# Performance work log

Measured on AMD Instinct MI355X. Metric: run time of the kernel, lower is better.

Reference implementation:

```python
import jax, jax.numpy as jnp
import numpy as np

NEG = jnp.float32(-1e30)  # max-plus identity (finite to keep grads clean)


def setup_inputs() -> dict:
    key = jax.random.key(0)
    k1, k2 = jax.random.split(key)
    B, Cin, H, W = 8, 64, 64, 64
    Cout, kH, kW = 64, 3, 3
    x = jax.random.normal(k1, (B, Cin, H, W), dtype=jnp.float32)
    weight = jax.random.normal(k2, (Cout, Cin, kH, kW), dtype=jnp.float32)
    return {"x": x, "weight": weight, "kernel_size": 3, "padding": 1}


def reference(x, weight, kernel_size, padding):
    # Max-plus correlation (tropical conv), stride 1:
    #   out[b,co,y,x] = max_{ci,i,j} ( x_pad[b,ci,y+i,x+j] + weight[co,ci,i,j] )
    kH = kW = int(kernel_size)
    padH = padW = int(padding)
    B, Cin, H, W = x.shape
    Cout = weight.shape[0]
    xp = jnp.pad(x, ((0, 0), (0, 0), (padH, padH), (padW, padW)),
                 constant_values=NEG)  # -inf-like padding: identity of max
    Ho = H + 2 * padH - kH + 1
    Wo = W + 2 * padW - kW + 1
    out = jnp.full((B, Cout, Ho, Wo), NEG, dtype=x.dtype)
    for i in range(kH):          # small fixed kernel loop (kH*kW taps)
        for j in range(kW):
            win = xp[:, :, i:i + Ho, j:j + Wo]            # [B,Ci,Ho,Wo]
            cand = win[:, None] + weight[None, :, :, i, j, None, None]
            out = jnp.maximum(out, cand.max(axis=2))      # reduce over Ci
    return out
```

## Files before the change

### kernel.cpp

```cpp
#include <hip/hip_runtime.h>

#define NEGV -1e30f

constexpr int Bn = 8, Ci = 64, Hn = 64, Wn = 64, Co = 64;

constexpr int COB = 8;
constexpr int HT  = 4;

__global__ __launch_bounds__(256, 4)
void maxconv_kernel(const float* __restrict__ x, const float* __restrict__ wt,
                    float* __restrict__ out) {
    const int lane = threadIdx.x & 63;
    const int wrow = threadIdx.x >> 6;
    const int co0  = blockIdx.x * COB;
    const int h    = blockIdx.y * HT + wrow;
    const int b    = blockIdx.z;

    const int cl = lane > 0      ? lane - 1 : 0;
    const int cr = lane < Wn - 1 ? lane + 1 : Wn - 1;
    const bool edgeL = (lane == 0);
    const bool edgeR = (lane == Wn - 1);
    const bool hasUp = (h > 0);
    const bool hasDn = (h < Hn - 1);

    float acc[COB];
#pragma unroll
    for (int c = 0; c < COB; c++) acc[c] = NEGV;

    const float* p = x + ((size_t)b * Ci * Hn + h) * Wn;

    for (int ci = 0; ci < Ci; ci++, p += Hn * Wn) {
        float lm1 = NEGV, xm1 = NEGV, rm1 = NEGV;
        float lp1 = NEGV, xp1 = NEGV, rp1 = NEGV;
        if (hasUp) { lm1 = p[cl - Wn]; xm1 = p[lane - Wn]; rm1 = p[cr - Wn]; }
        if (hasDn) { lp1 = p[cl + Wn]; xp1 = p[lane + Wn]; rp1 = p[cr + Wn]; }
        float l0 = p[cl], x0 = p[lane], r0 = p[cr];

        if (edgeL) { lm1 = NEGV; l0 = NEGV; lp1 = NEGV; }
        if (edgeR) { rm1 = NEGV; r0 = NEGV; rp1 = NEGV; }

#pragma unroll
        for (int c = 0; c < COB; c++) {
            const float* wp = wt + ((size_t)(co0 + c) * Ci + ci) * 9;
            float t0 = lm1 + wp[0];
            float t1 = xm1 + wp[1];
            float t2 = rm1 + wp[2];
            float t3 = l0  + wp[3];
            float t4 = x0  + wp[4];
            float t5 = r0  + wp[5];
            float t6 = lp1 + wp[6];
            float t7 = xp1 + wp[7];
            float t8 = rp1 + wp[8];
            float a = acc[c];
            a = fmaxf(a, fmaxf(t0, t1));
            a = fmaxf(a, fmaxf(t2, t3));
            a = fmaxf(a, fmaxf(t4, t5));
            a = fmaxf(a, fmaxf(t6, t7));
            a = fmaxf(a, t8);
            acc[c] = a;
        }
    }

#pragma unroll
    for (int c = 0; c < COB; c++) {
        out[(((size_t)b * Co + co0 + c) * Hn + h) * Wn + lane] = acc[c];
    }
}

extern "C" void kernel_launch(void* const* d_in, const int* in_sizes, int n_in,
                              void* d_out, int out_size, void* d_ws, size_t ws_size,
                              hipStream_t stream) {
    const float* x  = (const float*)d_in[0];
    const float* wt = (const float*)d_in[1];
    float* out = (float*)d_out;

    dim3 grid(Co / COB, Hn / HT, Bn);
    maxconv_kernel<<<grid, 256, 0, stream>>>(x, wt, out);
}
```

Before: 125.4 us.

## Rewrite max-plus conv with weight pretranspose, double-buffered loads, max3 and XCD-aware grid

Adds a pre-pass kernel that repacks the weights so each channel group reads a contiguous block, plus a padding buffer of NEG values so the up and down border rows become branch-free pointer loads. The main kernel halves the channels per block to 4, software-pipelines the input and weight loads across pairs of input channels with sched barriers, reduces with v_max3_f32, and remaps block ids so that neighbouring blocks on one XCD share input rows. It also raises the occupancy hint. The cost is an extra kernel launch and twice as many blocks each re-reading the input.

```diff
diff --git a/kernel.cpp b/kernel.cpp
--- a/kernel.cpp
+++ b/kernel.cpp
@@ -4,67 +4,135 @@
 
 constexpr int Bn = 8, Ci = 64, Hn = 64, Wn = 64, Co = 64;
 
-constexpr int COB = 8;
-constexpr int HT  = 4;
+constexpr int COB = 4;
+constexpr int NG  = Co / COB;
+constexpr int WELEM = NG * Ci * COB * 9;
+constexpr int NEGN  = 64;
 
-__global__ __launch_bounds__(256, 4)
-void maxconv_kernel(const float* __restrict__ x, const float* __restrict__ wt,
-                    float* __restrict__ out) {
+__global__ __launch_bounds__(256)
+void wtrans_kernel(const float* __restrict__ wt, float* __restrict__ wT2) {
+    int idx = blockIdx.x * 256 + threadIdx.x;
+    if (idx < WELEM) {
+        int t  = idx % 36;
+        int cl = t / 9;
+        int k  = t % 9;
+        int ci = (idx / 36) % Ci;
+        int g  = idx / (36 * Ci);
+        wT2[idx] = wt[(((size_t)(g * COB + cl)) * Ci + ci) * 9 + k];
+    } else if (idx < WELEM + NEGN) {
+        wT2[idx] = NEGV;
+    }
+}
+
+__device__ __forceinline__ float vmax3(float a, float b, float c) {
+    float d;
+    asm("v_max3_f32 %0, %1, %2, %3" : "=v"(d) : "v"(a), "v"(b), "v"(c));
+    return d;
+}
+
+struct X9 { float um, uc, ur, cm, cc, cr, dm, dc, dr; };
+
+__device__ __forceinline__ void loadX(X9& x, const float* __restrict__ pu,
+                                      const float* __restrict__ pc,
+                                      const float* __restrict__ pd,
+                                      int cl, int lane, int cr2) {
+    x.um = pu[cl]; x.uc = pu[lane]; x.ur = pu[cr2];
+    x.cm = pc[cl]; x.cc = pc[lane]; x.cr = pc[cr2];
+    x.dm = pd[cl]; x.dc = pd[lane]; x.dr = pd[cr2];
+}
+
+__device__ __forceinline__ void edgefix(X9& x, bool eL, bool eR) {
+    x.um = eL ? NEGV : x.um;  x.cm = eL ? NEGV : x.cm;  x.dm = eL ? NEGV : x.dm;
+    x.ur = eR ? NEGV : x.ur;  x.cr = eR ? NEGV : x.cr;  x.dr = eR ? NEGV : x.dr;
+}
+
+__device__ __forceinline__ void loadW(float* wv, const float* __restrict__ base) {
+#pragma unroll
+    for (int j = 0; j < 36; j++) wv[j] = base[j];
+}
+
+__device__ __forceinline__ void computeC(float* acc, const X9& x, const float* wv) {
+#pragma unroll
+    for (int c = 0; c < COB; c++) {
+        const float* w = wv + c * 9;
+        float t0 = x.um + w[0], t1 = x.uc + w[1], t2 = x.ur + w[2];
+        float t3 = x.cm + w[3], t4 = x.cc + w[4], t5 = x.cr + w[5];
+        float t6 = x.dm + w[6], t7 = x.dc + w[7], t8 = x.dr + w[8];
+        float m0 = vmax3(t0, t1, t2);
+        float m1 = vmax3(t3, t4, t5);
+        float m2 = vmax3(t6, t7, t8);
+        acc[c] = vmax3(acc[c], m0, m1);
+        acc[c] = fmaxf(acc[c], m2);
+    }
+}
+
+__global__ __launch_bounds__(256, 8)
+void maxconv_main(const float* __restrict__ x, const float* __restrict__ wT2,
+                  float* __restrict__ out) {
     const int lane = threadIdx.x & 63;
-    const int wrow = threadIdx.x >> 6;
-    const int co0  = blockIdx.x * COB;
-    const int h    = blockIdx.y * HT + wrow;
-    const int b    = blockIdx.z;
+    const int wid  = __builtin_amdgcn_readfirstlane(threadIdx.x >> 6);
 
-    const int cl = lane > 0      ? lane - 1 : 0;
-    const int cr = lane < Wn - 1 ? lane + 1 : Wn - 1;
-    const bool edgeL = (lane == 0);
-    const bool edgeR = (lane == Wn - 1);
-    const bool hasUp = (h > 0);
-    const bool hasDn = (h < Hn - 1);
+    const int id  = blockIdx.x;
+    const int xcd = id & 7;
+    const int g   = (id >> 3) & 15;
+    const int c   = xcd | ((id >> 7) << 3);
+    const int b   = c >> 4;
+    const int h   = (c & 15) * 4 + wid;
+
+    const int  cl  = lane > 0      ? lane - 1 : 0;
+    const int  cr2 = lane < Wn - 1 ? lane + 1 : Wn - 1;
+    const bool eL  = (lane == 0);
+    const bool eR  = (lane == Wn - 1);
+
+    const float* negbuf = wT2 + WELEM;
+
+    const bool hasUp = (h > 0), hasDn = (h < Hn - 1);
+    const float* pc = x + (((size_t)b * Ci) * Hn + h) * Wn;
+    const float* pu = hasUp ? pc - Wn : negbuf;
+    const float* pd = hasDn ? pc + Wn : negbuf;
+    const int sU = hasUp ? Hn * Wn : 0;
+    const int sC = Hn * Wn;
+    const int sD = hasDn ? Hn * Wn : 0;
+
+    const float* wrow = wT2 + (size_t)g * Ci * 36;
 
     float acc[COB];
 #pragma unroll
-    for (int c = 0; c < COB; c++) acc[c] = NEGV;
+    for (int q = 0; q < COB; q++) acc[q] = NEGV;
 
-    const float* p = x + ((size_t)b * Ci * Hn + h) * Wn;
+    X9 xA, xB;
+    float wvA[36], wvB[36];
 
-    for (int ci = 0; ci < Ci; ci++, p += Hn * Wn) {
-        float lm1 = NEGV, xm1 = NEGV, rm1 = NEGV;
-        float lp1 = NEGV, xp1 = NEGV, rp1 = NEGV;
-        if (hasUp) { lm1 = p[cl - Wn]; xm1 = p[lane - Wn]; rm1 = p[cr - Wn]; }
-        if (hasDn) { lp1 = p[cl + Wn]; xp1 = p[lane + Wn]; rp1 = p[cr + Wn]; }
-        float l0 = p[cl], x0 = p[lane], r0 = p[cr];
+    loadX(xA, pu, pc, pd, cl, lane, cr2);
+    pu += sU; pc += sC; pd += sD;
 
-        if (edgeL) { lm1 = NEGV; l0 = NEGV; lp1 = NEGV; }
-        if (edgeR) { rm1 = NEGV; r0 = NEGV; rp1 = NEGV; }
+#pragma unroll 1
+    for (int ci = 0; ci < Ci - 2; ci += 2) {
+        loadX(xB, pu, pc, pd, cl, lane, cr2);
+        pu += sU; pc += sC; pd += sD;
+        loadW(wvA, wrow);
+        loadW(wvB, wrow + 36);
+        wrow += 72;
+        __builtin_amdgcn_sched_barrier(0);
+        edgefix(xA, eL, eR);
+        computeC(acc, xA, wvA);
+        loadX(xA, pu, pc, pd, cl, lane, cr2);
+        pu += sU; pc += sC; pd += sD;
+        __builtin_amdgcn_sched_barrier(0);
+        edgefix(xB, eL, eR);
+        computeC(acc, xB, wvB);
+    }
+    loadX(xB, pu, pc, pd, cl, lane, cr2);
+    loadW(wvA, wrow);
+    loadW(wvB, wrow + 36);
+    edgefix(xA, eL, eR);
+    computeC(acc, xA, wvA);
+    edgefix(xB, eL, eR);
+    computeC(acc, xB, wvB);
 
+    float* po = out + (((size_t)b * Co + g * COB) * Hn + h) * Wn + lane;
 #pragma unroll
-        for (int c = 0; c < COB; c++) {
-            const float* wp = wt + ((size_t)(co0 + c) * Ci + ci) * 9;
-            float t0 = lm1 + wp[0];
-            float t1 = xm1 + wp[1];
-            float t2 = rm1 + wp[2];
-            float t3 = l0  + wp[3];
-            float t4 = x0  + wp[4];
-            float t5 = r0  + wp[5];
-            float t6 = lp1 + wp[6];
-            float t7 = xp1 + wp[7];
-            float t8 = rp1 + wp[8];
-            float a = acc[c];
-            a = fmaxf(a, fmaxf(t0, t1));
-            a = fmaxf(a, fmaxf(t2, t3));
-            a = fmaxf(a, fmaxf(t4, t5));
-            a = fmaxf(a, fmaxf(t6, t7));
-            a = fmaxf(a, t8);
-            acc[c] = a;
-        }
-    }
-
-#pragma unroll
-    for (int c = 0; c < COB; c++) {
-        out[(((size_t)b * Co + co0 + c) * Hn + h) * Wn + lane] = acc[c];
-    }
+    for (int q = 0; q < COB; q++) po[(size_t)q * Hn * Wn] = acc[q];
 }
 
 extern "C" void kernel_launch(void* const* d_in, const int* in_sizes, int n_in,
@@ -73,7 +141,9 @@
     const float* x  = (const float*)d_in[0];
     const float* wt = (const float*)d_in[1];
     float* out = (float*)d_out;
+    float* wT2 = (float*)d_ws;
 
-    dim3 grid(Co / COB, Hn / HT, Bn);
-    maxconv_kernel<<<grid, 256, 0, stream>>>(x, wt, out);
+    wtrans_kernel<<<(WELEM + NEGN + 255) / 256, 256, 0, stream>>>(wt, wT2);
+
+    maxconv_main<<<2048, 256, 0, stream>>>(x, wT2, out);
 }
```

Measured after the change: 176.5 us. +40.8%, slower.
